# Performance work log

Hardware: AMD Instinct MI355X
Metric: run time of the kernel (lower is better)

## Reference

```python
import jax, jax.numpy as jnp
import numpy as np

B, S, D, H, DFF = 2, 4096, 256, 8, 1024
DK = D // H


def setup_inputs() -> dict:
    key = jax.random.key(0)
    ks = jax.random.split(key, 12)
    sc = 0.02
    inp = {
        "x": jax.random.normal(ks[0], (B, S, D), jnp.float32),
        "mask": jnp.ones((B, 1, 1, S), jnp.int32),
        "Wq": jax.random.normal(ks[1], (D, D), jnp.float32) * sc,
        "bq": jnp.zeros((D,), jnp.float32),
        "Wk": jax.random.normal(ks[2], (D, D), jnp.float32) * sc,
        "bk": jnp.zeros((D,), jnp.float32),
        "Wv": jax.random.normal(ks[3], (D, D), jnp.float32) * sc,
        "bv": jnp.zeros((D,), jnp.float32),
        "Wo": jax.random.normal(ks[4], (D, D), jnp.float32) * sc,
        "bo": jnp.zeros((D,), jnp.float32),
        "W1": jax.random.normal(ks[5], (D, DFF), jnp.float32) * sc,
        "b1": jnp.zeros((DFF,), jnp.float32),
        "W2": jax.random.normal(ks[6], (DFF, D), jnp.float32) * sc,
        "b2": jnp.zeros((D,), jnp.float32),
        "g1": jnp.ones((D,), jnp.float32),
        "be1": jnp.zeros((D,), jnp.float32),
        "g2": jnp.ones((D,), jnp.float32),
        "be2": jnp.zeros((D,), jnp.float32),
        "a1": jnp.float32(1e-8),
        "a2": jnp.float32(1e-8),
    }
    return inp


def _layernorm(x, g, b, eps=1e-5):
    mu = jnp.mean(x, axis=-1, keepdims=True)
    var = jnp.var(x, axis=-1, keepdims=True)
    return (x - mu) * jax.lax.rsqrt(var + eps) * g + b


def _block(x, mask, Wq, bq, Wk, bk, Wv, bv, Wo, bo, W1, b1, W2, b2, g1, be1, g2, be2, a1, a2):
    # multi-head attention (dropout = identity in eval)
    def proj(W, b):
        return (x @ W + b).reshape(B, S, H, DK).transpose(0, 2, 1, 3)  # [B,H,S,DK]
    q, k, v = proj(Wq, bq), proj(Wk, bk), proj(Wv, bv)
    scores = jnp.einsum("bhsd,bhtd->bhst", q, k) / jnp.sqrt(jnp.float32(DK))
    scores = jnp.where(mask == 0, jnp.float32(-1e9), scores)
    p_attn = jax.nn.softmax(scores, axis=-1)
    ctx = jnp.einsum("bhst,bhtd->bhsd", p_attn, v)
    ctx = ctx.transpose(0, 2, 1, 3).reshape(B, S, D)
    attn_out = ctx @ Wo + bo
    x1 = _layernorm(x + a1 * attn_out, g1, be1)
    # FFN
    h = jax.nn.gelu(x1 @ W1 + b1, approximate=False)
    ffn_out = h @ W2 + b2
    return _layernorm(x1 + a2 * ffn_out, g2, be2)


def reference(x, mask, Wq, bq, Wk, bk, Wv, bv, Wo, bo, W1, b1, W2, b2, g1, be1, g2, be2, a1, a2):
    return _block(x, mask, Wq, bq, Wk, bk, Wv, bv, Wo, bo, W1, b1, W2, b2, g1, be1, g2, be2, a1, a2)
```

## Files before the change

### kernel.cpp

```cpp
#include <hip/hip_runtime.h>
#include <hip/hip_bf16.h>
#include <math.h>

#define B_ 2
#define S_ 4096
#define D_ 256
#define H_ 8
#define DFF_ 1024
#define DK_ 32

typedef __attribute__((ext_vector_type(8))) short short8;
typedef __attribute__((ext_vector_type(4))) float f32x4;
typedef __attribute__((ext_vector_type(16))) float f32x16;
typedef __attribute__((ext_vector_type(4))) int int4v;

__device__ __forceinline__ unsigned short f2bf(float f) {
  unsigned int u = __builtin_bit_cast(unsigned int, f);
  u += 0x7FFFu + ((u >> 16) & 1u);
  return (unsigned short)(u >> 16);
}

__device__ __forceinline__ float bf2f(unsigned short s) {
  unsigned int u = ((unsigned int)s) << 16;
  return __builtin_bit_cast(float, u);
}

__device__ __forceinline__ short8 u32x4_to_s8(unsigned int a, unsigned int b,
                                              unsigned int c, unsigned int d) {
  int4v v = {(int)a, (int)b, (int)c, (int)d};
  return __builtin_bit_cast(short8, v);
}

__device__ __forceinline__ float gelu_fast(float v) {
  float e = __builtin_amdgcn_exp2f(v * fmaf(0.10294609f, v * v, 2.3022077f));
  float th = 1.0f - 2.0f * __builtin_amdgcn_rcpf(e + 1.0f);
  return 0.5f * v * (1.0f + th);
}

__global__ __launch_bounds__(256) void k_prepw(
    const float* __restrict__ Wq, const float* __restrict__ Wk,
    const float* __restrict__ Wv, const float* __restrict__ Wo,
    const float* __restrict__ W1, const float* __restrict__ W2,
    const float* __restrict__ bq, const float* __restrict__ bk,
    const float* __restrict__ bv, const float* __restrict__ x,
    unsigned short* __restrict__ WqkvT, unsigned short* __restrict__ WoT,
    unsigned short* __restrict__ W1T, unsigned short* __restrict__ W2T,
    float* __restrict__ bqkv, unsigned short* __restrict__ xb) {
  const float k2 = 0.25500525551f;
  int bx = blockIdx.x, t = threadIdx.x;

  if (bx < 192) {
    __shared__ float tile[64][65];
    const float* src;
    unsigned short* dst;
    int Ksz, Nsz, ti, tj;
    float scale = 1.0f;
    if (bx < 48) {
      int which = bx >> 4, s = bx & 15;
      src = (which == 0) ? Wq : (which == 1) ? Wk : Wv;
      dst = WqkvT + which * 65536;
      Ksz = 256; Nsz = 256; ti = s >> 2; tj = s & 3;
      if (which == 0) scale = k2;
    } else if (bx < 64) {
      int s = bx - 48;
      src = Wo; dst = WoT; Ksz = 256; Nsz = 256; ti = s >> 2; tj = s & 3;
    } else if (bx < 128) {
      int s = bx - 64;
      src = W1; dst = W1T; Ksz = 256; Nsz = 1024; ti = s >> 4; tj = s & 15;
    } else {
      int s = bx - 128;
      src = W2; dst = W2T; Ksz = 1024; Nsz = 256; ti = s >> 2; tj = s & 3;
    }
    int row0 = ti * 64, col0 = tj * 64;
    int c = t & 63, rg = t >> 6;
#pragma unroll
    for (int i = 0; i < 16; i++) {
      int rr = rg * 16 + i;
      tile[rr][c] = src[(size_t)(row0 + rr) * Nsz + col0 + c] * scale;
    }
    __syncthreads();
    int k = t & 63;
#pragma unroll
    for (int i = 0; i < 16; i++) {
      int nn = rg * 16 + i;
      dst[(size_t)(col0 + nn) * Ksz + row0 + k] = f2bf(tile[k][nn]);
    }
  } else if (bx == 192) {
#pragma unroll
    for (int j = 0; j < 3; j++) {
      int i = j * 256 + t;
      if (i < 768)
        bqkv[i] = (i < 256) ? bq[i] * k2 : (i < 512) ? bk[i - 256] : bv[i - 512];
    }
  } else {
    int i = (bx - 193) * 2048 + t * 8;
    f32x4 f0 = *(const f32x4*)(x + i);
    f32x4 f1 = *(const f32x4*)(x + i + 4);
    short8 o;
#pragma unroll
    for (int e = 0; e < 4; e++) { o[e] = (short)f2bf(f0[e]); o[e + 4] = (short)f2bf(f1[e]); }
    *(short8*)(xb + i) = o;
  }
}

__global__ __launch_bounds__(256) void k_gemmqkv(const unsigned short* __restrict__ A,
                                                 const unsigned short* __restrict__ Bt,
                                                 const float* __restrict__ bias,
                                                 unsigned short* __restrict__ qb,
                                                 unsigned short* __restrict__ kpk,
                                                 unsigned short* __restrict__ vpk) {
  const int K = 256;
  __shared__ unsigned short Al[128][40];
  __shared__ unsigned short Bl[128][40];
  const int tid = threadIdx.x;
  const int wid = tid >> 6, lane = tid & 63;
  const int lhi = lane >> 4, llo = lane & 15;
  const int wr = wid >> 1, wc = wid & 1;
  const int rowbase = wr * 64, colbase = wc * 64;
  const int bm = blockIdx.x, bn = blockIdx.y;

  f32x4 zero = {0.f, 0.f, 0.f, 0.f};
  f32x4 acc[4][4];
#pragma unroll
  for (int m = 0; m < 4; m++)
#pragma unroll
    for (int n = 0; n < 4; n++) acc[m][n] = zero;

  const int r0 = tid >> 2, c8 = (tid & 3) * 8;
  const unsigned short* A16a = A + (size_t)(bm * 128 + r0) * K + c8;
  const unsigned short* A16b = A + (size_t)(bm * 128 + r0 + 64) * K + c8;
  const unsigned short* Brow0 = Bt + (size_t)(bn * 128 + r0) * K + c8;
  const unsigned short* Brow1 = Bt + (size_t)(bn * 128 + r0 + 64) * K + c8;

  for (int kb = 0; kb < K; kb += 32) {
    __syncthreads();
    *(short8*)&Al[r0][c8] = *(const short8*)(A16a + kb);
    *(short8*)&Al[r0 + 64][c8] = *(const short8*)(A16b + kb);
    *(short8*)&Bl[r0][c8] = *(const short8*)(Brow0 + kb);
    *(short8*)&Bl[r0 + 64][c8] = *(const short8*)(Brow1 + kb);
    __syncthreads();
    short8 af[4], bf[4];
#pragma unroll
    for (int m = 0; m < 4; m++) af[m] = *(const short8*)&Al[rowbase + m * 16 + llo][lhi * 8];
#pragma unroll
    for (int n = 0; n < 4; n++) bf[n] = *(const short8*)&Bl[colbase + n * 16 + llo][lhi * 8];
#pragma unroll
    for (int m = 0; m < 4; m++)
#pragma unroll
      for (int n = 0; n < 4; n++)
        acc[m][n] = __builtin_amdgcn_mfma_f32_16x16x32_bf16(af[m], bf[n], acc[m][n], 0, 0, 0);
  }

#pragma unroll
  for (int m = 0; m < 4; m++)
#pragma unroll
    for (int n = 0; n < 4; n++)
#pragma unroll
      for (int r = 0; r < 4; r++) {
        int row = bm * 128 + rowbase + m * 16 + lhi * 4 + r;
        int gcol = bn * 128 + colbase + n * 16 + llo;
        int which = gcol >> 8;
        int col0 = gcol & 255;
        float v = acc[m][n][r] + bias[gcol];
        unsigned short bv = f2bf(v);
        int t = row & (S_ - 1), b = row >> 12;
        int h = col0 >> 5;
        if (which == 0) {
          qb[(size_t)row * 256 + col0] = bv;
        } else if (which == 1) {
          int c5 = col0 & 31, jj = (c5 >> 4) & 1, hik = (c5 >> 3) & 1, e = c5 & 7;
          int tile = t >> 6, i = (t >> 5) & 1, l31k = t & 31;
          size_t addr = (((size_t)(b * 8 + h) * 64 + tile) * 4 + i * 2 + jj) * 512 +
                        (hik * 32 + l31k) * 8 + e;
          kpk[addr] = bv;
        } else {
          int d = col0 & 31;
          int x5 = t >> 6, j = (t >> 3) & 7, kk = t & 7;
          size_t addr = (((size_t)(b * 8 + h) * 64 + x5) * 4 + (j >> 1)) * 512 +
                        ((j & 1) * 32 + d) * 8 + kk;
          vpk[addr] = bv;
        }
      }
}

__global__ __launch_bounds__(256) void k_gemm1(const unsigned short* __restrict__ A,
                                               const unsigned short* __restrict__ Bt,
                                               const float* __restrict__ bias,
                                               unsigned short* __restrict__ Cout,
                                               int M, int N, int K) {
  __shared__ unsigned short Al[128][40];
  __shared__ unsigned short Bl[128][40];
  const int tid = threadIdx.x;
  const int wid = tid >> 6, lane = tid & 63;
  const int lhi = lane >> 4, llo = lane & 15;
  const int wr = wid >> 1, wc = wid & 1;
  const int rowbase = wr * 64, colbase = wc * 64;
  const int bm = blockIdx.x, bn = blockIdx.y;

  f32x4 zero = {0.f, 0.f, 0.f, 0.f};
  f32x4 acc[4][4];
#pragma unroll
  for (int m = 0; m < 4; m++)
#pragma unroll
    for (int n = 0; n < 4; n++) acc[m][n] = zero;

  const int r0 = tid >> 2, c8 = (tid & 3) * 8;
  const unsigned short* A16a = A + (size_t)(bm * 128 + r0) * K + c8;
  const unsigned short* A16b = A + (size_t)(bm * 128 + r0 + 64) * K + c8;
  const unsigned short* Brow0 = Bt + (size_t)(bn * 128 + r0) * K + c8;
  const unsigned short* Brow1 = Bt + (size_t)(bn * 128 + r0 + 64) * K + c8;

  for (int kb = 0; kb < K; kb += 32) {
    __syncthreads();
    *(short8*)&Al[r0][c8] = *(const short8*)(A16a + kb);
    *(short8*)&Al[r0 + 64][c8] = *(const short8*)(A16b + kb);
    *(short8*)&Bl[r0][c8] = *(const short8*)(Brow0 + kb);
    *(short8*)&Bl[r0 + 64][c8] = *(const short8*)(Brow1 + kb);
    __syncthreads();
    short8 af[4], bf[4];
#pragma unroll
    for (int m = 0; m < 4; m++) af[m] = *(const short8*)&Al[rowbase + m * 16 + llo][lhi * 8];
#pragma unroll
    for (int n = 0; n < 4; n++) bf[n] = *(const short8*)&Bl[colbase + n * 16 + llo][lhi * 8];
#pragma unroll
    for (int m = 0; m < 4; m++)
#pragma unroll
      for (int n = 0; n < 4; n++)
        acc[m][n] = __builtin_amdgcn_mfma_f32_16x16x32_bf16(af[m], bf[n], acc[m][n], 0, 0, 0);
  }

#pragma unroll
  for (int m = 0; m < 4; m++)
#pragma unroll
    for (int n = 0; n < 4; n++)
#pragma unroll
      for (int r = 0; r < 4; r++) {
        int row = bm * 128 + rowbase + m * 16 + lhi * 4 + r;
        int col = bn * 128 + colbase + n * 16 + llo;
        float v = acc[m][n][r] + bias[col];
        Cout[(size_t)row * N + col] = f2bf(gelu_fast(v));
      }
}

template <int BASE16, int OUT32>
__global__ __launch_bounds__(512) void k_gemmln(const unsigned short* __restrict__ A,
                                                const unsigned short* __restrict__ Bt,
                                                const float* __restrict__ bias,
                                                const void* __restrict__ base,
                                                const float* __restrict__ alpha,
                                                const float* __restrict__ g,
                                                const float* __restrict__ be,
                                                void* __restrict__ y, int K) {
  __shared__ unsigned short Al[2][32][40];
  __shared__ unsigned short Bl[2][256][40];
  __shared__ float psum[32][4], psq[32][4];
  float* partial = (float*)&Bl[0][0][0];

  const int tid = threadIdx.x;
  const int w = tid >> 6, lane = tid & 63;
  const int kh = w >> 2, wc = w & 3;
  const int lhi = lane >> 4, llo = lane & 15;
  const int row0 = blockIdx.x * 32;
  const int Kh = K >> 1;

  f32x4 zero = {0.f, 0.f, 0.f, 0.f};
  f32x4 acc[2][4];
#pragma unroll
  for (int m = 0; m < 2; m++)
#pragma unroll
    for (int n = 0; n < 4; n++) acc[m][n] = zero;

  for (int kb = 0; kb < Kh; kb += 32) {
    __syncthreads();
    if (tid < 256) {
      int kh2 = tid >> 7, ra = (tid >> 2) & 31, ca = (tid & 3) * 8;
      *(short8*)&Al[kh2][ra][ca] =
          *(const short8*)(A + (size_t)(row0 + ra) * K + kh2 * Kh + kb + ca);
    }
#pragma unroll
    for (int s = 0; s < 4; s++) {
      int c = tid + s * 512;
      int kh2 = c >> 10, rb = (c >> 2) & 255, cb = (c & 3) * 8;
      *(short8*)&Bl[kh2][rb][cb] =
          *(const short8*)(Bt + (size_t)rb * K + kh2 * Kh + kb + cb);
    }
    __syncthreads();
    short8 af[2], bf[4];
#pragma unroll
    for (int m = 0; m < 2; m++) af[m] = *(const short8*)&Al[kh][m * 16 + llo][lhi * 8];
#pragma unroll
    for (int n = 0; n < 4; n++)
      bf[n] = *(const short8*)&Bl[kh][wc * 64 + n * 16 + llo][lhi * 8];
#pragma unroll
    for (int m = 0; m < 2; m++)
#pragma unroll
      for (int n = 0; n < 4; n++)
        acc[m][n] = __builtin_amdgcn_mfma_f32_16x16x32_bf16(af[m], bf[n], acc[m][n], 0, 0, 0);
  }

  __syncthreads();
  if (kh == 1) {
#pragma unroll
    for (int m = 0; m < 2; m++)
#pragma unroll
      for (int n = 0; n < 4; n++)
#pragma unroll
        for (int r = 0; r < 4; r++) {
          int lrow = m * 16 + lhi * 4 + r;
          int col = wc * 64 + n * 16 + llo;
          partial[lrow * 256 + col] = acc[m][n][r];
        }
  }
  __syncthreads();

  const float a = alpha[0];
  const unsigned short* b16 = (const unsigned short*)base;
  const float* b32 = (const float*)base;

  if (kh == 0) {
#pragma unroll
    for (int m = 0; m < 2; m++)
#pragma unroll
      for (int r = 0; r < 4; r++) {
        int lrow = m * 16 + lhi * 4 + r;
        size_t grow = (size_t)(row0 + lrow);
        float s = 0.f, q = 0.f;
#pragma unroll
        for (int n = 0; n < 4; n++) {
          int col = wc * 64 + n * 16 + llo;
          float v = acc[m][n][r] + partial[lrow * 256 + col] + bias[col];
          float xb = BASE16 ? bf2f(b16[grow * 256 + col]) : b32[grow * 256 + col];
          float rr = fmaf(a, v, xb);
          acc[m][n][r] = rr;
          s += rr;
          q = fmaf(rr, rr, q);
        }
#pragma unroll
        for (int off = 1; off < 16; off <<= 1) {
          s += __shfl_xor(s, off);
          q += __shfl_xor(q, off);
        }
        if (llo == 0) { psum[lrow][wc] = s; psq[lrow][wc] = q; }
      }
  }
  __syncthreads();

  if (kh == 0) {
#pragma unroll
    for (int m = 0; m < 2; m++)
#pragma unroll
      for (int r = 0; r < 4; r++) {
        int lrow = m * 16 + lhi * 4 + r;
        size_t grow = (size_t)(row0 + lrow);
        float S = psum[lrow][0] + psum[lrow][1] + psum[lrow][2] + psum[lrow][3];
        float Q = psq[lrow][0] + psq[lrow][1] + psq[lrow][2] + psq[lrow][3];
        float mu = S * (1.0f / 256.0f);
        float var = Q * (1.0f / 256.0f) - mu * mu;
        float rs = rsqrtf(var + 1e-5f);
#pragma unroll
        for (int n = 0; n < 4; n++) {
          int col = wc * 64 + n * 16 + llo;
          float o = (acc[m][n][r] - mu) * rs * g[col] + be[col];
          if (OUT32) ((float*)y)[grow * 256 + col] = o;
          else ((unsigned short*)y)[grow * 256 + col] = f2bf(o);
        }
      }
  }
}

__global__ __launch_bounds__(256, 2) void k_attn(const unsigned short* __restrict__ qbuf,
                                                 const unsigned short* __restrict__ kpk,
                                                 const unsigned short* __restrict__ vpk,
                                                 const int* __restrict__ mask,
                                                 unsigned short* __restrict__ ctx) {
  __shared__ float accS[4][64][32];
  __shared__ float lS[4][64];
  const int tid = threadIdx.x;
  const int lane = tid & 63;
  const int w = tid >> 6;
  const int l31 = lane & 31, hi = lane >> 5;
  const int q0 = blockIdx.x * 64;
  const int h = blockIdx.y, b = blockIdx.z;
  const size_t bS = (size_t)b * S_;

  const unsigned short* QpA = qbuf + (bS + q0 + l31) * 256 + h * DK_ + hi * 8;
  short8 qa0 = *(const short8*)QpA;
  short8 qa1 = *(const short8*)(QpA + 16);
  const unsigned short* QpB = QpA + 32 * 256;
  short8 qb0 = *(const short8*)QpB;
  short8 qb1 = *(const short8*)(QpB + 16);

  const size_t fragbase = ((size_t)(b * H_ + h) * 64 + w * 16) * 2048 + lane * 8;
  const unsigned short* kp = kpk + fragbase;
  const unsigned short* vp = vpk + fragbase;
  const int* mp = mask + bS + w * 1024 + lane;

  f32x16 accA, accB, laccA, laccB;
#pragma unroll
  for (int r = 0; r < 16; r++) { accA[r] = 0.f; accB[r] = 0.f; laccA[r] = 0.f; laccB[r] = 0.f; }
  const f32x16 zz = accA;
  short8 ones;
#pragma unroll
  for (int e = 0; e < 8; e++) ones[e] = (short)0x3F80;

  short8 kA[4], vA[4], kB[4], vB[4];
  unsigned int pk0[8], pk1[8];
  f32x16 s0, s1;
  int tcur = 0;
  int mvC, mvN;

#define LDK(DST) { DST[0] = *(const short8*)(kp); DST[1] = *(const short8*)(kp + 512); \
                   DST[2] = *(const short8*)(kp + 1024); DST[3] = *(const short8*)(kp + 1536); kp += 2048; }
#define LDV(DST) { DST[0] = *(const short8*)(vp); DST[1] = *(const short8*)(vp + 512); \
                   DST[2] = *(const short8*)(vp + 1024); DST[3] = *(const short8*)(vp + 1536); vp += 2048; }
#define QKM(KF, qx0, qx1) {                                                      \
    s0 = __builtin_amdgcn_mfma_f32_32x32x16_bf16(KF[0], qx0, zz, 0, 0, 0);       \
    s1 = __builtin_amdgcn_mfma_f32_32x32x16_bf16(KF[2], qx0, zz, 0, 0, 0);       \
    s0 = __builtin_amdgcn_mfma_f32_32x32x16_bf16(KF[1], qx1, s0, 0, 0, 0);       \
    s1 = __builtin_amdgcn_mfma_f32_32x32x16_bf16(KF[3], qx1, s1, 0, 0, 0);       \
  }
#define EXPM(bal) {                                                              \
    if (__builtin_expect((bal) != ~0ull, 0)) {                                   \
      _Pragma("unroll") for (int r = 0; r < 16; r++) {                           \
        int tt = (r & 3) + 8 * (r >> 2) + 4 * hi;                                \
        if (!(((bal) >> tt) & 1)) s0[r] = -3e38f;                                \
        if (!(((bal) >> (tt + 32)) & 1)) s1[r] = -3e38f;                         \
      }                                                                          \
    }                                                                            \
    _Pragma("unroll") for (int r = 0; r < 16; r++) {                             \
      s0[r] = __builtin_amdgcn_exp2f(s0[r]);                                     \
      s1[r] = __builtin_amdgcn_exp2f(s1[r]);                                     \
    }                                                                            \
    _Pragma("unroll") for (int j = 0; j < 8; j++) {                              \
      asm("v_cvt_pk_bf16_f32 %0, %1, %2" : "=v"(pk0[j]) : "v"(s0[2*j]), "v"(s0[2*j+1])); \
      asm("v_cvt_pk_bf16_f32 %0, %1, %2" : "=v"(pk1[j]) : "v"(s1[2*j]), "v"(s1[2*j+1])); \
    }                                                                            \
  }
#define PVM(VF, accX, laccX) {                                                   \
    __builtin_amdgcn_s_setprio(1);                                               \
    _Pragma("unroll") for (int kk = 0; kk < 4; kk++) {                           \
      unsigned int* pk = (kk < 2) ? pk0 : pk1;                                   \
      int base = (kk & 1) * 4;                                                   \
      auto r02 = __builtin_amdgcn_permlane32_swap(pk[base], pk[base + 2], false, false);     \
      auto r13 = __builtin_amdgcn_permlane32_swap(pk[base + 1], pk[base + 3], false, false); \
      short8 pfr = u32x4_to_s8(r02[0], r13[0], r02[1], r13[1]);                  \
      accX = __builtin_amdgcn_mfma_f32_32x32x16_bf16(pfr, VF[kk], accX, 0, 0, 0);\
      laccX = __builtin_amdgcn_mfma_f32_32x32x16_bf16(pfr, ones, laccX, 0, 0, 0);\
    }                                                                            \
    __builtin_amdgcn_s_setprio(0);                                               \
  }
#define TILESTEP(KC, VC, KN, VN) {                                               \
    unsigned long long bal = __ballot(mvC != 0);                                 \
    QKM(KC, qa0, qa1);                                                           \
    LDK(KN);                                                                     \
    EXPM(bal);                                                                   \
    PVM(VC, accA, laccA);                                                        \
    QKM(KC, qb0, qb1);                                                           \
    LDV(VN);                                                                     \
    EXPM(bal);                                                                   \
    PVM(VC, accB, laccB);                                                        \
    mvC = mvN;                                                                   \
    tcur++;                                                                      \
    mvN = mp[(tcur + 1 < 16 ? tcur + 1 : 15) * 64];                              \
  }

  LDK(kA);
  LDV(vA);
  mvC = mp[0];
  mvN = mp[64];

  for (int it = 0; it < 8; ++it) {
    TILESTEP(kA, vA, kB, vB);
    TILESTEP(kB, vB, kA, vA);
  }

#pragma unroll
  for (int r = 0; r < 16; r++) {
    int q = (r & 3) + 8 * (r >> 2) + 4 * hi;
    accS[w][q][l31] = accA[r];
    accS[w][q + 32][l31] = accB[r];
  }
  if (l31 == 0) {
#pragma unroll
    for (int r = 0; r < 16; r++) {
      int q = (r & 3) + 8 * (r >> 2) + 4 * hi;
      lS[w][q] = laccA[r];
      lS[w][q + 32] = laccB[r];
    }
  }
  __syncthreads();
#pragma unroll
  for (int i = 0; i < 8; i++) {
    int e = tid + 256 * i;
    int q = e >> 5, d = e & 31;
    float o = accS[0][q][d] + accS[1][q][d] + accS[2][q][d] + accS[3][q][d];
    float L = lS[0][q] + lS[1][q] + lS[2][q] + lS[3][q];
    ctx[(bS + q0 + q) * (size_t)D_ + h * DK_ + d] = f2bf(o / L);
  }
#undef LDK
#undef LDV
#undef QKM
#undef EXPM
#undef PVM
#undef TILESTEP
}

extern "C" void kernel_launch(void* const* d_in, const int* in_sizes, int n_in,
                              void* d_out, int out_size, void* d_ws, size_t ws_size,
                              hipStream_t stream) {
  const float* x   = (const float*)d_in[0];
  const int* mask  = (const int*)d_in[1];
  const float* Wq  = (const float*)d_in[2];
  const float* bq  = (const float*)d_in[3];
  const float* Wk  = (const float*)d_in[4];
  const float* bk  = (const float*)d_in[5];
  const float* Wv  = (const float*)d_in[6];
  const float* bv  = (const float*)d_in[7];
  const float* Wo  = (const float*)d_in[8];
  const float* bo  = (const float*)d_in[9];
  const float* W1  = (const float*)d_in[10];
  const float* b1  = (const float*)d_in[11];
  const float* W2  = (const float*)d_in[12];
  const float* b2  = (const float*)d_in[13];
  const float* g1  = (const float*)d_in[14];
  const float* be1 = (const float*)d_in[15];
  const float* g2  = (const float*)d_in[16];
  const float* be2 = (const float*)d_in[17];
  const float* a1  = (const float*)d_in[18];
  const float* a2  = (const float*)d_in[19];
  float* out = (float*)d_out;

  char* ws = (char*)d_ws;
  const size_t MB = 1024 * 1024;
  unsigned short* qb  = (unsigned short*)(ws + 0);
  unsigned short* kpk = (unsigned short*)(ws + 5 * MB);
  unsigned short* vpk = (unsigned short*)(ws + 10 * MB);
  unsigned short* ctx = (unsigned short*)(ws + 15 * MB);
  unsigned short* x1b = (unsigned short*)(ws + 19 * MB);
  unsigned short* hb  = (unsigned short*)(ws + 23 * MB);
  unsigned short* WqkvT = (unsigned short*)(ws + 40 * MB);
  unsigned short* WoT   = (unsigned short*)(ws + 40 * MB + 512 * 1024);
  unsigned short* W1T   = (unsigned short*)(ws + 41 * MB);
  unsigned short* W2T   = (unsigned short*)(ws + 41 * MB + 512 * 1024);
  float* bqkv           = (float*)(ws + 42 * MB);
  unsigned short* xb    = (unsigned short*)(ws + 43 * MB);

  const int NTOK = B_ * S_;

  k_prepw<<<dim3(1217), 256, 0, stream>>>(Wq, Wk, Wv, Wo, W1, W2, bq, bk, bv, x,
                                          WqkvT, WoT, W1T, W2T, bqkv, xb);

  k_gemmqkv<<<dim3(64, 6), 256, 0, stream>>>(xb, WqkvT, bqkv, qb, kpk, vpk);

  k_attn<<<dim3(S_ / 64, H_, B_), 256, 0, stream>>>(qb, kpk, vpk, mask, ctx);

  k_gemmln<0, 0><<<dim3(NTOK / 32), 512, 0, stream>>>(ctx, WoT, bo, x, a1, g1, be1,
                                                      x1b, 256);

  k_gemm1<<<dim3(64, 8), 256, 0, stream>>>(x1b, W1T, b1, hb, NTOK, 1024, 256);

  k_gemmln<1, 1><<<dim3(NTOK / 32), 512, 0, stream>>>(hb, W2T, b2, x1b, a2, g2, be2,
                                                      out, 1024);
}
```

Measured before the change: 123.3 us.

## Fuse FFN up-projection, GELU, down-projection and LayerNorm into one kernel

Replaces the separate W1 GEMM+GELU kernel and the W2 GEMM+LayerNorm kernel with a single per-32-row kernel. The 1024-wide hidden activation is produced in 256-column chunks, staged only in LDS, and consumed immediately by the second GEMM, so the bf16 hidden tensor never goes to global memory. W1 and W2 are prepacked into an MFMA-fragment layout so B operands can be loaded straight from global memory per lane without LDS staging. In exchange, each block re-reads all of W1 and W2 from L2 with no LDS reuse across waves, and with only 32 rows per block the MFMA work per weight byte is low.

```diff
diff --git a/kernel.cpp b/kernel.cpp
--- a/kernel.cpp
+++ b/kernel.cpp
@@ -44,7 +44,7 @@
     const float* __restrict__ bq, const float* __restrict__ bk,
     const float* __restrict__ bv, const float* __restrict__ x,
     unsigned short* __restrict__ WqkvT, unsigned short* __restrict__ WoT,
-    unsigned short* __restrict__ W1T, unsigned short* __restrict__ W2T,
+    unsigned short* __restrict__ W1pk, unsigned short* __restrict__ W2pk,
     float* __restrict__ bqkv, unsigned short* __restrict__ xb) {
   const float k2 = 0.25500525551f;
   int bx = blockIdx.x, t = threadIdx.x;
@@ -52,24 +52,22 @@
   if (bx < 192) {
     __shared__ float tile[64][65];
     const float* src;
-    unsigned short* dst;
-    int Ksz, Nsz, ti, tj;
+    int Nsz, ti, tj;
     float scale = 1.0f;
     if (bx < 48) {
       int which = bx >> 4, s = bx & 15;
       src = (which == 0) ? Wq : (which == 1) ? Wk : Wv;
-      dst = WqkvT + which * 65536;
-      Ksz = 256; Nsz = 256; ti = s >> 2; tj = s & 3;
+      Nsz = 256; ti = s >> 2; tj = s & 3;
       if (which == 0) scale = k2;
     } else if (bx < 64) {
       int s = bx - 48;
-      src = Wo; dst = WoT; Ksz = 256; Nsz = 256; ti = s >> 2; tj = s & 3;
+      src = Wo; Nsz = 256; ti = s >> 2; tj = s & 3;
     } else if (bx < 128) {
       int s = bx - 64;
-      src = W1; dst = W1T; Ksz = 256; Nsz = 1024; ti = s >> 4; tj = s & 15;
+      src = W1; Nsz = 1024; ti = s >> 4; tj = s & 15;
     } else {
       int s = bx - 128;
-      src = W2; dst = W2T; Ksz = 1024; Nsz = 256; ti = s >> 2; tj = s & 3;
+      src = W2; Nsz = 256; ti = s >> 2; tj = s & 3;
     }
     int row0 = ti * 64, col0 = tj * 64;
     int c = t & 63, rg = t >> 6;
@@ -79,11 +77,33 @@
       tile[rr][c] = src[(size_t)(row0 + rr) * Nsz + col0 + c] * scale;
     }
     __syncthreads();
-    int k = t & 63;
-#pragma unroll
-    for (int i = 0; i < 16; i++) {
-      int nn = rg * 16 + i;
-      dst[(size_t)(col0 + nn) * Ksz + row0 + k] = f2bf(tile[k][nn]);
+
+    if (bx < 64) {
+      unsigned short* dst;
+      if (bx < 48) dst = WqkvT + (bx >> 4) * 65536;
+      else dst = WoT;
+      int k = t & 63;
+#pragma unroll
+      for (int i = 0; i < 16; i++) {
+        int nn = rg * 16 + i;
+        dst[(size_t)(col0 + nn) * 256 + row0 + k] = f2bf(tile[k][nn]);
+      }
+    } else {
+      unsigned short* pk = (bx < 128) ? W1pk : W2pk;
+      int kst_tot = (bx < 128) ? 8 : 32;
+      int lane2 = t & 63, sub2 = t >> 6;
+#pragma unroll
+      for (int i = 0; i < 2; i++) {
+        int subc = sub2 * 2 + i;
+        int ntl = subc >> 1, kst = subc & 1;
+        short8 o;
+#pragma unroll
+        for (int e = 0; e < 8; e++)
+          o[e] = (short)f2bf(tile[kst * 32 + (lane2 >> 4) * 8 + e][ntl * 16 + (lane2 & 15)]);
+        int ntg = tj * 4 + ntl;
+        int ksg = ti * 2 + kst;
+        *(short8*)(pk + ((size_t)(ntg * kst_tot + ksg) * 64 + lane2) * 8) = o;
+      }
     }
   } else if (bx == 192) {
 #pragma unroll
@@ -183,63 +203,125 @@
       }
 }
 
-__global__ __launch_bounds__(256) void k_gemm1(const unsigned short* __restrict__ A,
-                                               const unsigned short* __restrict__ Bt,
-                                               const float* __restrict__ bias,
-                                               unsigned short* __restrict__ Cout,
-                                               int M, int N, int K) {
-  __shared__ unsigned short Al[128][40];
-  __shared__ unsigned short Bl[128][40];
+__global__ __launch_bounds__(512) void k_ffn(const unsigned short* __restrict__ x1b,
+                                             const unsigned short* __restrict__ W1pk,
+                                             const float* __restrict__ b1,
+                                             const unsigned short* __restrict__ W2pk,
+                                             const float* __restrict__ b2,
+                                             const float* __restrict__ alpha,
+                                             const float* __restrict__ g,
+                                             const float* __restrict__ be,
+                                             float* __restrict__ out) {
+  __shared__ unsigned short Ax[32][268];
+  __shared__ unsigned short Hl[32][268];
+  __shared__ float psum[32][8], psq[32][8];
   const int tid = threadIdx.x;
-  const int wid = tid >> 6, lane = tid & 63;
+  const int w = tid >> 6, lane = tid & 63;
   const int lhi = lane >> 4, llo = lane & 15;
-  const int wr = wid >> 1, wc = wid & 1;
-  const int rowbase = wr * 64, colbase = wc * 64;
-  const int bm = blockIdx.x, bn = blockIdx.y;
-
-  f32x4 zero = {0.f, 0.f, 0.f, 0.f};
-  f32x4 acc[4][4];
-#pragma unroll
-  for (int m = 0; m < 4; m++)
-#pragma unroll
-    for (int n = 0; n < 4; n++) acc[m][n] = zero;
-
-  const int r0 = tid >> 2, c8 = (tid & 3) * 8;
-  const unsigned short* A16a = A + (size_t)(bm * 128 + r0) * K + c8;
-  const unsigned short* A16b = A + (size_t)(bm * 128 + r0 + 64) * K + c8;
-  const unsigned short* Brow0 = Bt + (size_t)(bn * 128 + r0) * K + c8;
-  const unsigned short* Brow1 = Bt + (size_t)(bn * 128 + r0 + 64) * K + c8;
-
-  for (int kb = 0; kb < K; kb += 32) {
+  const int row0 = blockIdx.x * 32;
+
+  {
+    int r = tid >> 4, c0 = (tid & 15) * 16;
+    const unsigned short* src = x1b + (size_t)(row0 + r) * 256 + c0;
+    *(short8*)&Ax[r][c0] = *(const short8*)(src);
+    *(short8*)&Ax[r][c0 + 8] = *(const short8*)(src + 8);
+  }
+  __syncthreads();
+
+  f32x4 zero4 = {0.f, 0.f, 0.f, 0.f};
+  f32x4 acc2[2][2];
+#pragma unroll
+  for (int m = 0; m < 2; m++)
+#pragma unroll
+    for (int n = 0; n < 2; n++) acc2[m][n] = zero4;
+
+  for (int c = 0; c < 4; ++c) {
+    f32x4 acc1[2][2];
+#pragma unroll
+    for (int m = 0; m < 2; m++)
+#pragma unroll
+      for (int n = 0; n < 2; n++) acc1[m][n] = zero4;
+    const unsigned short* w1base = W1pk + (size_t)(c * 16 + w * 2) * 4096 + lane * 8;
+#pragma unroll
+    for (int kb = 0; kb < 8; ++kb) {
+      short8 af0 = *(const short8*)&Ax[llo][kb * 32 + lhi * 8];
+      short8 af1 = *(const short8*)&Ax[16 + llo][kb * 32 + lhi * 8];
+      short8 bf0 = *(const short8*)(w1base + kb * 512);
+      short8 bf1 = *(const short8*)(w1base + 4096 + kb * 512);
+      acc1[0][0] = __builtin_amdgcn_mfma_f32_16x16x32_bf16(af0, bf0, acc1[0][0], 0, 0, 0);
+      acc1[0][1] = __builtin_amdgcn_mfma_f32_16x16x32_bf16(af0, bf1, acc1[0][1], 0, 0, 0);
+      acc1[1][0] = __builtin_amdgcn_mfma_f32_16x16x32_bf16(af1, bf0, acc1[1][0], 0, 0, 0);
+      acc1[1][1] = __builtin_amdgcn_mfma_f32_16x16x32_bf16(af1, bf1, acc1[1][1], 0, 0, 0);
+    }
     __syncthreads();
-    *(short8*)&Al[r0][c8] = *(const short8*)(A16a + kb);
-    *(short8*)&Al[r0 + 64][c8] = *(const short8*)(A16b + kb);
-    *(short8*)&Bl[r0][c8] = *(const short8*)(Brow0 + kb);
-    *(short8*)&Bl[r0 + 64][c8] = *(const short8*)(Brow1 + kb);
+#pragma unroll
+    for (int m = 0; m < 2; m++)
+#pragma unroll
+      for (int n = 0; n < 2; n++)
+#pragma unroll
+        for (int r = 0; r < 4; r++) {
+          int col = w * 32 + n * 16 + llo;
+          float v = acc1[m][n][r] + b1[c * 256 + col];
+          Hl[m * 16 + lhi * 4 + r][col] = f2bf(gelu_fast(v));
+        }
     __syncthreads();
-    short8 af[4], bf[4];
-#pragma unroll
-    for (int m = 0; m < 4; m++) af[m] = *(const short8*)&Al[rowbase + m * 16 + llo][lhi * 8];
-#pragma unroll
-    for (int n = 0; n < 4; n++) bf[n] = *(const short8*)&Bl[colbase + n * 16 + llo][lhi * 8];
-#pragma unroll
-    for (int m = 0; m < 4; m++)
-#pragma unroll
-      for (int n = 0; n < 4; n++)
-        acc[m][n] = __builtin_amdgcn_mfma_f32_16x16x32_bf16(af[m], bf[n], acc[m][n], 0, 0, 0);
-  }
-
-#pragma unroll
-  for (int m = 0; m < 4; m++)
-#pragma unroll
-    for (int n = 0; n < 4; n++)
-#pragma unroll
-      for (int r = 0; r < 4; r++) {
-        int row = bm * 128 + rowbase + m * 16 + lhi * 4 + r;
-        int col = bn * 128 + colbase + n * 16 + llo;
-        float v = acc[m][n][r] + bias[col];
-        Cout[(size_t)row * N + col] = f2bf(gelu_fast(v));
-      }
+    const unsigned short* w2base = W2pk + (size_t)(w * 2) * 16384 + (size_t)(c * 8) * 512 + lane * 8;
+#pragma unroll
+    for (int kk = 0; kk < 8; ++kk) {
+      short8 a0 = *(const short8*)&Hl[llo][kk * 32 + lhi * 8];
+      short8 a1 = *(const short8*)&Hl[16 + llo][kk * 32 + lhi * 8];
+      short8 bf0 = *(const short8*)(w2base + kk * 512);
+      short8 bf1 = *(const short8*)(w2base + 16384 + kk * 512);
+      acc2[0][0] = __builtin_amdgcn_mfma_f32_16x16x32_bf16(a0, bf0, acc2[0][0], 0, 0, 0);
+      acc2[0][1] = __builtin_amdgcn_mfma_f32_16x16x32_bf16(a0, bf1, acc2[0][1], 0, 0, 0);
+      acc2[1][0] = __builtin_amdgcn_mfma_f32_16x16x32_bf16(a1, bf0, acc2[1][0], 0, 0, 0);
+      acc2[1][1] = __builtin_amdgcn_mfma_f32_16x16x32_bf16(a1, bf1, acc2[1][1], 0, 0, 0);
+    }
+  }
+
+  const float a = alpha[0];
+#pragma unroll
+  for (int m = 0; m < 2; m++)
+#pragma unroll
+    for (int r = 0; r < 4; r++) {
+      int lrow = m * 16 + lhi * 4 + r;
+      float s = 0.f, q = 0.f;
+#pragma unroll
+      for (int n = 0; n < 2; n++) {
+        int col = w * 32 + n * 16 + llo;
+        float v = acc2[m][n][r] + b2[col];
+        float xv = bf2f(Ax[lrow][col]);
+        float rr = fmaf(a, v, xv);
+        acc2[m][n][r] = rr;
+        s += rr;
+        q = fmaf(rr, rr, q);
+      }
+#pragma unroll
+      for (int off = 1; off < 16; off <<= 1) {
+        s += __shfl_xor(s, off);
+        q += __shfl_xor(q, off);
+      }
+      if (llo == 0) { psum[lrow][w] = s; psq[lrow][w] = q; }
+    }
+  __syncthreads();
+#pragma unroll
+  for (int m = 0; m < 2; m++)
+#pragma unroll
+    for (int r = 0; r < 4; r++) {
+      int lrow = m * 16 + lhi * 4 + r;
+      size_t grow = (size_t)(row0 + lrow);
+      float S = 0.f, Q = 0.f;
+#pragma unroll
+      for (int j = 0; j < 8; j++) { S += psum[lrow][j]; Q += psq[lrow][j]; }
+      float mu = S * (1.0f / 256.0f);
+      float var = Q * (1.0f / 256.0f) - mu * mu;
+      float rs = rsqrtf(var + 1e-5f);
+#pragma unroll
+      for (int n = 0; n < 2; n++) {
+        int col = w * 32 + n * 16 + llo;
+        out[grow * 256 + col] = (acc2[m][n][r] - mu) * rs * g[col] + be[col];
+      }
+    }
 }
 
 template <int BASE16, int OUT32>
@@ -537,18 +619,17 @@
   unsigned short* vpk = (unsigned short*)(ws + 10 * MB);
   unsigned short* ctx = (unsigned short*)(ws + 15 * MB);
   unsigned short* x1b = (unsigned short*)(ws + 19 * MB);
-  unsigned short* hb  = (unsigned short*)(ws + 23 * MB);
   unsigned short* WqkvT = (unsigned short*)(ws + 40 * MB);
   unsigned short* WoT   = (unsigned short*)(ws + 40 * MB + 512 * 1024);
-  unsigned short* W1T   = (unsigned short*)(ws + 41 * MB);
-  unsigned short* W2T   = (unsigned short*)(ws + 41 * MB + 512 * 1024);
+  unsigned short* W1pk  = (unsigned short*)(ws + 41 * MB);
+  unsigned short* W2pk  = (unsigned short*)(ws + 41 * MB + 512 * 1024);
   float* bqkv           = (float*)(ws + 42 * MB);
   unsigned short* xb    = (unsigned short*)(ws + 43 * MB);
 
   const int NTOK = B_ * S_;
 
   k_prepw<<<dim3(1217), 256, 0, stream>>>(Wq, Wk, Wv, Wo, W1, W2, bq, bk, bv, x,
-                                          WqkvT, WoT, W1T, W2T, bqkv, xb);
+                                          WqkvT, WoT, W1pk, W2pk, bqkv, xb);
 
   k_gemmqkv<<<dim3(64, 6), 256, 0, stream>>>(xb, WqkvT, bqkv, qb, kpk, vpk);
 
@@ -557,8 +638,5 @@
   k_gemmln<0, 0><<<dim3(NTOK / 32), 512, 0, stream>>>(ctx, WoT, bo, x, a1, g1, be1,
                                                       x1b, 256);
 
-  k_gemm1<<<dim3(64, 8), 256, 0, stream>>>(x1b, W1T, b1, hb, NTOK, 1024, 256);
-
-  k_gemmln<1, 1><<<dim3(NTOK / 32), 512, 0, stream>>>(hb, W2T, b2, x1b, a2, g2, be2,
-                                                      out, 1024);
-}
+  k_ffn<<<dim3(NTOK / 32), 512, 0, stream>>>(x1b, W1pk, b1, W2pk, b2, a2, g2, be2, out);
+}
```

Result: faster. 112.5 us (-8.8%).
